# Kernel tuning notes

Hardware: AMD Instinct MI355X
Metric: run time of the kernel (lower is better)

## Reference

```python
import jax, jax.numpy as jnp
import numpy as np

B, T, C = 32, 2048, 1024  # batch, seq_len (<= block_size), n_embd
HEAD_SIZE = 128


def setup_inputs() -> dict:
    key = jax.random.key(0)
    kx, kk, kq, kv = jax.random.split(key, 4)
    std = 0.02  # CustomLinear init: normal(0, 0.02)
    return {
        "x": jax.random.normal(kx, (B, T, C), dtype=jnp.float32),
        "Wk": jax.random.normal(kk, (HEAD_SIZE, C), dtype=jnp.float32) * std,
        "Wq": jax.random.normal(kq, (HEAD_SIZE, C), dtype=jnp.float32) * std,
        "Wv": jax.random.normal(kv, (HEAD_SIZE, C), dtype=jnp.float32) * std,
    }


def reference(x, Wk, Wq, Wv):
    # x: [B, T, C]; W*: [head_size, C] (torch Linear layout, no bias)
    Bb, Tt, Cc = x.shape
    k = jnp.einsum("btc,hc->bth", x, Wk)
    q = jnp.einsum("btc,hc->bth", x, Wq)
    v = jnp.einsum("btc,hc->bth", x, Wv)
    # NOTE: original scales by C**-0.5 (n_embd), not head_size**-0.5
    wei = jnp.einsum("bth,bsh->bts", q, k) * (Cc ** -0.5)
    causal = jnp.tril(jnp.ones((Tt, Tt), dtype=bool))  # tril[:T,:T]
    wei = jnp.where(causal, wei, -jnp.inf)
    wei = jax.nn.softmax(wei, axis=-1)
    return jnp.einsum("bts,bsh->bth", wei, v)  # [B, T, head_size]
```

## Files before the change

### kernel.cpp

```cpp
#include <hip/hip_runtime.h>
#include <hip/hip_bf16.h>

typedef __bf16 bf8_t __attribute__((ext_vector_type(8)));
typedef __bf16 bf4_t __attribute__((ext_vector_type(4)));
typedef float f4_t __attribute__((ext_vector_type(4)));

#define B_ 32
#define T_ 2048
#define C_ 1024
#define H_ 128

__global__ __launch_bounds__(256) void wconv_kernel(
    const float* __restrict__ Wk, const float* __restrict__ Wq, const float* __restrict__ Wv,
    __bf16* __restrict__ Wr)
{
    const int e  = (blockIdx.x * 256 + threadIdx.x) * 8;
    const int kk = e & 31;
    const int lr = (e >> 5) & 15;
    const int ks = (e >> 9) & 31;
    const int cg = e >> 14;
    const int col = cg * 16 + lr;
    const int k   = ks * 32 + kk;
    const float* W = (col < 128) ? Wk : (col < 256) ? Wq : Wv;
    const float* p = W + (size_t)(col & 127) * C_ + k;
    float4 f0 = *(const float4*)p;
    float4 f1 = *(const float4*)(p + 4);
    bf8_t o;
    o[0] = (__bf16)f0.x; o[1] = (__bf16)f0.y; o[2] = (__bf16)f0.z; o[3] = (__bf16)f0.w;
    o[4] = (__bf16)f1.x; o[5] = (__bf16)f1.y; o[6] = (__bf16)f1.z; o[7] = (__bf16)f1.w;
    *(bf8_t*)(Wr + e) = o;
}

__global__ __launch_bounds__(512, 4) void proj_kernel(
    const float* __restrict__ x, const __bf16* __restrict__ Wr,
    __bf16* __restrict__ Kb, __bf16* __restrict__ Qb, __bf16* __restrict__ VtG)
{
    __shared__ __bf16 Xs[2][64][136];

    const int m0   = blockIdx.x * 64;
    const int tid  = threadIdx.x;
    const int lane = tid & 63;
    const int w    = tid >> 6;
    const int wm   = w >> 2;
    const int wn   = w & 3;
    const int lr   = lane & 15;
    const int quad = lane >> 4;

    const int r0 = tid >> 5;
    const int c4 = (tid & 31) << 2;

    f4_t acc[2][6];
    #pragma unroll
    for (int mi = 0; mi < 2; mi++)
        #pragma unroll
        for (int ni = 0; ni < 6; ni++) acc[mi][ni] = f4_t{0.f, 0.f, 0.f, 0.f};

    float4 pf[4];

#define LOADC(c) { _Pragma("unroll") \
    for (int i_ = 0; i_ < 4; ++i_) \
        pf[i_] = *(const float4*)(x + (size_t)(m0 + r0 + i_ * 16) * C_ + (c) * 128 + c4); }

#define WRITEC(bsel) { _Pragma("unroll") \
    for (int i_ = 0; i_ < 4; ++i_) { \
        float4 f_ = pf[i_]; \
        *(bf4_t*)&Xs[bsel][r0 + i_ * 16][c4] = \
            bf4_t{(__bf16)f_.x, (__bf16)f_.y, (__bf16)f_.z, (__bf16)f_.w}; } }

#define COMPUTE(c, bsel) { _Pragma("unroll") \
    for (int k4_ = 0; k4_ < 4; ++k4_) { \
        bf8_t xa_[2]; \
        _Pragma("unroll") \
        for (int mi = 0; mi < 2; ++mi) \
            xa_[mi] = *(const bf8_t*)&Xs[bsel][wm * 32 + mi * 16 + lr][k4_ * 32 + quad * 8]; \
        _Pragma("unroll") \
        for (int ni = 0; ni < 6; ++ni) { \
            bf8_t wb_ = *(const bf8_t*)(Wr + (size_t)((ni * 4 + wn) * 32 + (c) * 4 + k4_) * 512 + lr * 32 + quad * 8); \
            if (ni < 4) { \
                _Pragma("unroll") \
                for (int mi = 0; mi < 2; ++mi) \
                    acc[mi][ni] = __builtin_amdgcn_mfma_f32_16x16x32_bf16(xa_[mi], wb_, acc[mi][ni], 0, 0, 0); \
            } else { \
                _Pragma("unroll") \
                for (int mi = 0; mi < 2; ++mi) \
                    acc[mi][ni] = __builtin_amdgcn_mfma_f32_16x16x32_bf16(wb_, xa_[mi], acc[mi][ni], 0, 0, 0); \
            } } } }

    LOADC(0)
    WRITEC(0)
    __syncthreads();

    #pragma unroll
    for (int c = 0; c < 8; ++c) {
        if (c < 7) LOADC(c + 1)
        COMPUTE(c, c & 1)
        if (c < 7) {
            WRITEC((c + 1) & 1)
            __syncthreads();
        }
    }

#undef LOADC
#undef WRITEC
#undef COMPUTE

    const int bb = m0 >> 11;
    const int t0 = m0 & (T_ - 1);
    #pragma unroll
    for (int ni = 0; ni < 4; ni++) {
        __bf16* Out = (ni < 2) ? Kb : Qb;
        const int col = (ni & 1) * 64 + wn * 16 + lr;
        #pragma unroll
        for (int mi = 0; mi < 2; mi++)
            for (int r = 0; r < 4; r++) {
                const int row = m0 + wm * 32 + mi * 16 + quad * 4 + r;
                Out[(size_t)row * H_ + col] = (__bf16)acc[mi][ni][r];
            }
    }
    #pragma unroll
    for (int ni = 4; ni < 6; ni++)
        for (int mi = 0; mi < 2; mi++) {
            const int tok = t0 + wm * 32 + mi * 16 + lr;
            #pragma unroll
            for (int r = 0; r < 4; r++) {
                const int h = (ni - 4) * 64 + wn * 16 + quad * 4 + r;
                VtG[(size_t)bb * H_ * T_ + (size_t)h * T_ + tok] = (__bf16)acc[mi][ni][r];
            }
        }
}

__global__ __launch_bounds__(512, 4) void flash_kernel(
    const __bf16* __restrict__ Qb, const __bf16* __restrict__ Kb,
    const __bf16* __restrict__ VtG, float* __restrict__ Out)
{
    __shared__ __bf16 Ks[64][136];
    __shared__ __bf16 Vt[128][72];
    __shared__ __bf16 Ps[128][72];

    const int qt = (blockIdx.y < 16) ? (15 - blockIdx.x) : blockIdx.x;
    const int b  = blockIdx.y;
    const size_t kqbase = (size_t)b * T_ * H_;
    const size_t vbase  = (size_t)b * H_ * T_;

    const int tid  = threadIdx.x;
    const int lane = tid & 63;
    const int w    = tid >> 6;
    const int lr   = lane & 15;
    const int quad = lane >> 4;

    bf8_t qf[4];
    {
        const __bf16* qp = Qb + kqbase + (size_t)(qt * 128 + w * 16 + lr) * H_ + quad * 8;
        #pragma unroll
        for (int ks = 0; ks < 4; ks++) qf[ks] = *(const bf8_t*)(qp + ks * 32);
    }

    f4_t o[8];
    #pragma unroll
    for (int n = 0; n < 8; n++) o[n] = f4_t{0.f, 0.f, 0.f, 0.f};
    float ls[4] = {0.f, 0.f, 0.f, 0.f};

    const float sc = 0.03125f * 1.4426950408889634f;
    const int jmax = 2 * qt + 1;

    const int kRow0 = tid >> 4,          kC0 = (tid & 15) << 3;
    const int kRow1 = (tid + 512) >> 4,  kC1 = ((tid + 512) & 15) << 3;
    const int vH0 = tid >> 3,            vS0 = (tid & 7) << 3;
    const int vH1 = (tid + 512) >> 3,    vS1 = ((tid + 512) & 7) << 3;

    bf8_t kr0 = *(const bf8_t*)(Kb + kqbase + (size_t)kRow0 * H_ + kC0);
    bf8_t kr1 = *(const bf8_t*)(Kb + kqbase + (size_t)kRow1 * H_ + kC1);
    bf8_t vr0 = *(const bf8_t*)(VtG + vbase + (size_t)vH0 * T_ + vS0);
    bf8_t vr1 = *(const bf8_t*)(VtG + vbase + (size_t)vH1 * T_ + vS1);

    for (int j = 0; j <= jmax; j++) {
        __syncthreads();
        *(bf8_t*)&Ks[kRow0][kC0] = kr0;
        *(bf8_t*)&Ks[kRow1][kC1] = kr1;
        *(bf8_t*)&Vt[vH0][vS0]   = vr0;
        *(bf8_t*)&Vt[vH1][vS1]   = vr1;
        __syncthreads();
        if (j < jmax) {
            const int s0 = (j + 1) * 64;
            kr0 = *(const bf8_t*)(Kb + kqbase + (size_t)(s0 + kRow0) * H_ + kC0);
            kr1 = *(const bf8_t*)(Kb + kqbase + (size_t)(s0 + kRow1) * H_ + kC1);
            vr0 = *(const bf8_t*)(VtG + vbase + (size_t)vH0 * T_ + s0 + vS0);
            vr1 = *(const bf8_t*)(VtG + vbase + (size_t)vH1 * T_ + s0 + vS1);
        }
        if (j == jmax && w < 4) continue;

        f4_t s4[4];
        #pragma unroll
        for (int n = 0; n < 4; n++) s4[n] = f4_t{0.f, 0.f, 0.f, 0.f};
        #pragma unroll
        for (int ks = 0; ks < 4; ks++)
            for (int n = 0; n < 4; n++) {
                bf8_t kf = *(const bf8_t*)&Ks[n * 16 + lr][ks * 32 + quad * 8];
                s4[n] = __builtin_amdgcn_mfma_f32_16x16x32_bf16(qf[ks], kf, s4[n], 0, 0, 0);
            }

        const bool domask = (j - 2 * qt) == (w >> 2);
        const int rowg = qt * 128 + w * 16 + quad * 4;
        #pragma unroll
        for (int n = 0; n < 4; n++) {
            const int colg = j * 64 + n * 16 + lr;
            #pragma unroll
            for (int r = 0; r < 4; r++) {
                float p = __builtin_exp2f(s4[n][r] * sc);
                if (domask && colg > rowg + r) p = 0.f;
                ls[r] += p;
                Ps[w * 16 + quad * 4 + r][n * 16 + lr] = (__bf16)p;
            }
        }

        #pragma unroll
        for (int ks = 0; ks < 2; ks++) {
            bf8_t pf = *(const bf8_t*)&Ps[w * 16 + lr][ks * 32 + quad * 8];
            #pragma unroll
            for (int n = 0; n < 8; n++) {
                bf8_t vf = *(const bf8_t*)&Vt[n * 16 + lr][ks * 32 + quad * 8];
                o[n] = __builtin_amdgcn_mfma_f32_16x16x32_bf16(pf, vf, o[n], 0, 0, 0);
            }
        }
    }

    float inv[4];
    #pragma unroll
    for (int r = 0; r < 4; r++) {
        float v = ls[r];
        v += __shfl_xor(v, 1);
        v += __shfl_xor(v, 2);
        v += __shfl_xor(v, 4);
        v += __shfl_xor(v, 8);
        inv[r] = 1.f / v;
    }
    #pragma unroll
    for (int n = 0; n < 8; n++) {
        const int col = n * 16 + lr;
        #pragma unroll
        for (int r = 0; r < 4; r++) {
            const int row = qt * 128 + w * 16 + quad * 4 + r;
            Out[kqbase + (size_t)row * H_ + col] = o[n][r] * inv[r];
        }
    }
}

extern "C" void kernel_launch(void* const* d_in, const int* in_sizes, int n_in,
                              void* d_out, int out_size, void* d_ws, size_t ws_size,
                              hipStream_t stream) {
    const float* x  = (const float*)d_in[0];
    const float* Wk = (const float*)d_in[1];
    const float* Wq = (const float*)d_in[2];
    const float* Wv = (const float*)d_in[3];
    float* out = (float*)d_out;

    const size_t n_kqv = (size_t)B_ * T_ * H_;
    __bf16* Kb  = (__bf16*)d_ws;
    __bf16* Qb  = Kb + n_kqv;
    __bf16* VtG = Qb + n_kqv;
    __bf16* Wr  = VtG + n_kqv;

    wconv_kernel<<<dim3(192), 256, 0, stream>>>(Wk, Wq, Wv, Wr);
    proj_kernel<<<dim3((B_ * T_) / 64), 512, 0, stream>>>(x, Wr, Kb, Qb, VtG);
    flash_kernel<<<dim3(16, B_), 512, 0, stream>>>(Qb, Kb, VtG, out);
}
```

Before: 511.3 us.

## Retile projection GEMM into 128x128 per-head tiles with LDS-staged weights

The QKV projection kernel is restructured so each 256-thread block computes a 128-row by 128-column tile for one of K, Q or V, instead of 64 rows across all 384 columns. Weight chunks are now staged into double-buffered shared memory with global_load_lds rather than read directly from global memory by every wave. The x tile is stored in an XOR-swizzled layout to avoid bank conflicts. The intent is more MFMA reuse per loaded fragment and less global weight traffic, at the cost of each x row being read and converted three times, once per head block.

```diff
diff --git a/kernel.cpp b/kernel.cpp
--- a/kernel.cpp
+++ b/kernel.cpp
@@ -31,102 +31,130 @@
     *(bf8_t*)(Wr + e) = o;
 }
 
-__global__ __launch_bounds__(512, 4) void proj_kernel(
+__global__ __launch_bounds__(256) void proj_kernel(
     const float* __restrict__ x, const __bf16* __restrict__ Wr,
     __bf16* __restrict__ Kb, __bf16* __restrict__ Qb, __bf16* __restrict__ VtG)
 {
-    __shared__ __bf16 Xs[2][64][136];
-
-    const int m0   = blockIdx.x * 64;
+    __shared__ __bf16 As[128 * 64];
+    __shared__ __bf16 Bs[2][16 * 512];
+
+    const int nt   = blockIdx.x % 3;
+    const int m0   = (blockIdx.x / 3) * 128;
     const int tid  = threadIdx.x;
     const int lane = tid & 63;
     const int w    = tid >> 6;
-    const int wm   = w >> 2;
-    const int wn   = w & 3;
+    const int wqm  = w >> 1;
+    const int wqn  = w & 1;
     const int lr   = lane & 15;
     const int quad = lane >> 4;
 
-    const int r0 = tid >> 5;
-    const int c4 = (tid & 31) << 2;
-
-    f4_t acc[2][6];
-    #pragma unroll
-    for (int mi = 0; mi < 2; mi++)
-        #pragma unroll
-        for (int ni = 0; ni < 6; ni++) acc[mi][ni] = f4_t{0.f, 0.f, 0.f, 0.f};
-
-    float4 pf[4];
-
-#define LOADC(c) { _Pragma("unroll") \
-    for (int i_ = 0; i_ < 4; ++i_) \
-        pf[i_] = *(const float4*)(x + (size_t)(m0 + r0 + i_ * 16) * C_ + (c) * 128 + c4); }
-
-#define WRITEC(bsel) { _Pragma("unroll") \
+    f4_t acc[4][4];
+    #pragma unroll
+    for (int mi = 0; mi < 4; mi++)
+        #pragma unroll
+        for (int ni = 0; ni < 4; ni++) acc[mi][ni] = f4_t{0.f, 0.f, 0.f, 0.f};
+
+    float4 pf[8];
+
+#define LOADA(t) { _Pragma("unroll") \
+    for (int i_ = 0; i_ < 8; ++i_) { \
+        const int u_ = i_ * 256 + tid; \
+        pf[i_] = *(const float4*)(x + (size_t)(m0 + (u_ >> 4)) * C_ + (t) * 64 + (u_ & 15) * 4); } }
+
+#define WRITEA { _Pragma("unroll") \
+    for (int i_ = 0; i_ < 8; ++i_) { \
+        const int u_ = i_ * 256 + tid; \
+        const int r_ = u_ >> 4; \
+        float4 f_ = pf[i_]; \
+        *(bf4_t*)&As[r_ * 64 + ((((u_ & 15) * 4)) ^ ((r_ & 7) * 8))] = \
+            bf4_t{(__bf16)f_.x, (__bf16)f_.y, (__bf16)f_.z, (__bf16)f_.w}; } }
+
+#define STAGEB(t, bsel) { _Pragma("unroll") \
     for (int i_ = 0; i_ < 4; ++i_) { \
-        float4 f_ = pf[i_]; \
-        *(bf4_t*)&Xs[bsel][r0 + i_ * 16][c4] = \
-            bf4_t{(__bf16)f_.x, (__bf16)f_.y, (__bf16)f_.z, (__bf16)f_.w}; } }
-
-#define COMPUTE(c, bsel) { _Pragma("unroll") \
-    for (int k4_ = 0; k4_ < 4; ++k4_) { \
-        bf8_t xa_[2]; \
-        _Pragma("unroll") \
-        for (int mi = 0; mi < 2; ++mi) \
-            xa_[mi] = *(const bf8_t*)&Xs[bsel][wm * 32 + mi * 16 + lr][k4_ * 32 + quad * 8]; \
-        _Pragma("unroll") \
-        for (int ni = 0; ni < 6; ++ni) { \
-            bf8_t wb_ = *(const bf8_t*)(Wr + (size_t)((ni * 4 + wn) * 32 + (c) * 4 + k4_) * 512 + lr * 32 + quad * 8); \
-            if (ni < 4) { \
-                _Pragma("unroll") \
-                for (int mi = 0; mi < 2; ++mi) \
-                    acc[mi][ni] = __builtin_amdgcn_mfma_f32_16x16x32_bf16(xa_[mi], wb_, acc[mi][ni], 0, 0, 0); \
-            } else { \
-                _Pragma("unroll") \
-                for (int mi = 0; mi < 2; ++mi) \
-                    acc[mi][ni] = __builtin_amdgcn_mfma_f32_16x16x32_bf16(wb_, xa_[mi], acc[mi][ni], 0, 0, 0); \
-            } } } }
-
-    LOADC(0)
-    WRITEC(0)
+        const int ci_ = i_ * 4 + w; \
+        const __bf16* src_ = Wr + ((size_t)((nt * 8 + (ci_ >> 1)) * 32 + (t) * 2 + (ci_ & 1)) << 9) + lane * 8; \
+        __builtin_amdgcn_global_load_lds( \
+            (const __attribute__((address_space(1))) void*)src_, \
+            (__attribute__((address_space(3))) void*)&Bs[bsel][ci_ << 9], 16, 0, 0); } }
+
+    LOADA(0)
+    STAGEB(0, 0)
+    WRITEA
     __syncthreads();
 
-    #pragma unroll
-    for (int c = 0; c < 8; ++c) {
-        if (c < 7) LOADC(c + 1)
-        COMPUTE(c, c & 1)
-        if (c < 7) {
-            WRITEC((c + 1) & 1)
+    #pragma unroll 2
+    for (int t = 0; t < 16; ++t) {
+        const int bsel = t & 1;
+        if (t < 15) {
+            LOADA(t + 1)
+            STAGEB(t + 1, bsel ^ 1)
+        }
+        #pragma unroll
+        for (int kh = 0; kh < 2; ++kh) {
+            bf8_t af[4], bfr[4];
+            #pragma unroll
+            for (int mi = 0; mi < 4; ++mi) {
+                const int row = wqm * 64 + mi * 16 + lr;
+                af[mi] = *(const bf8_t*)&As[row * 64 + ((kh * 32 + quad * 8) ^ ((row & 7) * 8))];
+            }
+            #pragma unroll
+            for (int ni = 0; ni < 4; ++ni) {
+                const int ch = (wqn * 4 + ni) * 2 + kh;
+                bfr[ni] = *(const bf8_t*)&Bs[bsel][ch * 512 + lr * 32 + quad * 8];
+            }
+            if (nt < 2) {
+                #pragma unroll
+                for (int mi = 0; mi < 4; ++mi)
+                    #pragma unroll
+                    for (int ni = 0; ni < 4; ++ni)
+                        acc[mi][ni] = __builtin_amdgcn_mfma_f32_16x16x32_bf16(af[mi], bfr[ni], acc[mi][ni], 0, 0, 0);
+            } else {
+                #pragma unroll
+                for (int mi = 0; mi < 4; ++mi)
+                    #pragma unroll
+                    for (int ni = 0; ni < 4; ++ni)
+                        acc[mi][ni] = __builtin_amdgcn_mfma_f32_16x16x32_bf16(bfr[ni], af[mi], acc[mi][ni], 0, 0, 0);
+            }
+        }
+        __syncthreads();
+        if (t < 15) {
+            WRITEA
             __syncthreads();
         }
     }
 
-#undef LOADC
-#undef WRITEC
-#undef COMPUTE
-
-    const int bb = m0 >> 11;
-    const int t0 = m0 & (T_ - 1);
-    #pragma unroll
-    for (int ni = 0; ni < 4; ni++) {
-        __bf16* Out = (ni < 2) ? Kb : Qb;
-        const int col = (ni & 1) * 64 + wn * 16 + lr;
-        #pragma unroll
-        for (int mi = 0; mi < 2; mi++)
-            for (int r = 0; r < 4; r++) {
-                const int row = m0 + wm * 32 + mi * 16 + quad * 4 + r;
-                Out[(size_t)row * H_ + col] = (__bf16)acc[mi][ni][r];
-            }
-    }
-    #pragma unroll
-    for (int ni = 4; ni < 6; ni++)
-        for (int mi = 0; mi < 2; mi++) {
-            const int tok = t0 + wm * 32 + mi * 16 + lr;
-            #pragma unroll
-            for (int r = 0; r < 4; r++) {
-                const int h = (ni - 4) * 64 + wn * 16 + quad * 4 + r;
-                VtG[(size_t)bb * H_ * T_ + (size_t)h * T_ + tok] = (__bf16)acc[mi][ni][r];
-            }
-        }
+#undef LOADA
+#undef WRITEA
+#undef STAGEB
+
+    if (nt < 2) {
+        __bf16* Out = nt ? Qb : Kb;
+        #pragma unroll
+        for (int ni = 0; ni < 4; ++ni)
+            #pragma unroll
+            for (int mi = 0; mi < 4; ++mi) {
+                const int col = wqn * 64 + ni * 16 + lr;
+                #pragma unroll
+                for (int r = 0; r < 4; ++r) {
+                    const int row = m0 + wqm * 64 + mi * 16 + quad * 4 + r;
+                    Out[(size_t)row * H_ + col] = (__bf16)acc[mi][ni][r];
+                }
+            }
+    } else {
+        const int bb = m0 >> 11;
+        const int t0 = m0 & (T_ - 1);
+        #pragma unroll
+        for (int ni = 0; ni < 4; ++ni)
+            #pragma unroll
+            for (int mi = 0; mi < 4; ++mi) {
+                const int tok = t0 + wqm * 64 + mi * 16 + lr;
+                #pragma unroll
+                for (int r = 0; r < 4; ++r) {
+                    const int h = wqn * 64 + ni * 16 + quad * 4 + r;
+                    VtG[(size_t)bb * H_ * T_ + (size_t)h * T_ + tok] = (__bf16)acc[mi][ni][r];
+                }
+            }
+    }
 }
 
 __global__ __launch_bounds__(512, 4) void flash_kernel(
@@ -215,11 +243,11 @@
 
         #pragma unroll
         for (int ks = 0; ks < 2; ks++) {
-            bf8_t pf = *(const bf8_t*)&Ps[w * 16 + lr][ks * 32 + quad * 8];
+            bf8_t pf2 = *(const bf8_t*)&Ps[w * 16 + lr][ks * 32 + quad * 8];
             #pragma unroll
             for (int n = 0; n < 8; n++) {
                 bf8_t vf = *(const bf8_t*)&Vt[n * 16 + lr][ks * 32 + quad * 8];
-                o[n] = __builtin_amdgcn_mfma_f32_16x16x32_bf16(pf, vf, o[n], 0, 0, 0);
+                o[n] = __builtin_amdgcn_mfma_f32_16x16x32_bf16(pf2, vf, o[n], 0, 0, 0);
             }
         }
     }
@@ -261,6 +289,6 @@
     __bf16* Wr  = VtG + n_kqv;
 
     wconv_kernel<<<dim3(192), 256, 0, stream>>>(Wk, Wq, Wv, Wr);
-    proj_kernel<<<dim3((B_ * T_) / 64), 512, 0, stream>>>(x, Wr, Kb, Qb, VtG);
+    proj_kernel<<<dim3(512 * 3), 256, 0, stream>>>(x, Wr, Kb, Qb, VtG);
     flash_kernel<<<dim3(16, B_), 512, 0, stream>>>(Qb, Kb, VtG, out);
 }
```

Result: faster. 478.4 us (-6.4%).
